# Performance work log

Measured on AMD Instinct MI355X. Metric: run time of the kernel, lower is better.

## Reference

```python
import jax, jax.numpy as jnp
import numpy as np

EMBED_DIM = 1024
NUM_HEADS = 16
HEAD_DIM = EMBED_DIM // NUM_HEADS


def setup_inputs() -> dict:
    key = jax.random.key(0)
    k1, k2, k3, k4, k5 = jax.random.split(key, 5)
    B, S, D = 2, 2048, EMBED_DIM
    s_in = 1.0 / np.sqrt(D)
    x = jax.random.normal(k1, (B, S, D), dtype=jnp.float32)
    W_qkv = jax.random.uniform(k2, (D, 3 * D), dtype=jnp.float32, minval=-s_in, maxval=s_in)
    b_qkv = jax.random.uniform(k3, (3 * D,), dtype=jnp.float32, minval=-s_in, maxval=s_in)
    W_out = jax.random.uniform(k4, (D, D), dtype=jnp.float32, minval=-s_in, maxval=s_in)
    b_out = jax.random.uniform(k5, (D,), dtype=jnp.float32, minval=-s_in, maxval=s_in)
    return {"x": x, "W_qkv": W_qkv, "b_qkv": b_qkv, "W_out": W_out, "b_out": b_out}


def reference(x, W_qkv, b_qkv, W_out, b_out):
    B, S, D = x.shape
    H, Hd = NUM_HEADS, HEAD_DIM
    qkv = x @ W_qkv + b_qkv                      # [B,S,3D]
    qkv = qkv.reshape(B, S, 3, H, Hd)
    q = qkv[:, :, 0].transpose(0, 2, 1, 3)       # [B,H,S,Hd]
    k = qkv[:, :, 1].transpose(0, 2, 1, 3)
    v = qkv[:, :, 2].transpose(0, 2, 1, 3)
    scores = jnp.einsum('bhsd,bhtd->bhst', q, k) / jnp.sqrt(jnp.float32(Hd))
    attn = jax.nn.softmax(scores, axis=-1)       # dropout is identity in eval mode
    out = jnp.einsum('bhst,bhtd->bhsd', attn, v)
    out = out.transpose(0, 2, 1, 3).reshape(B, S, D)
    return out @ W_out + b_out
```

## Files before the change

### kernel.cpp

```cpp
#include <hip/hip_runtime.h>
#include <stdint.h>
#include <math.h>

#define EMBED 1024
#define HEADS 16
#define HDIM  64
#define SEQ   2048
#define BATCH 2

typedef __bf16 bf16x8 __attribute__((ext_vector_type(8)));
typedef float  f32x4  __attribute__((ext_vector_type(4)));
typedef unsigned short u16x8 __attribute__((ext_vector_type(8)));
typedef unsigned short u16x4 __attribute__((ext_vector_type(4)));
typedef uint32_t u32x4v __attribute__((ext_vector_type(4)));

static __device__ __forceinline__ unsigned short f2bf(float f){
  union { float f; uint32_t u; } v; v.f = f;
  uint32_t u = v.u;
  uint32_t r = (u + 0x7FFFu + ((u >> 16) & 1u)) >> 16;
  return (unsigned short)r;
}
static __device__ __forceinline__ bf16x8 as_bf(u16x8 v){ return __builtin_bit_cast(bf16x8, v); }

static __device__ __forceinline__ uint32_t pk_bf16(float a, float b){
#if defined(__has_builtin) && __has_builtin(__builtin_amdgcn_cvt_pk_bf16_f32)
  typedef __bf16 bf16x2 __attribute__((ext_vector_type(2)));
  bf16x2 p = __builtin_amdgcn_cvt_pk_bf16_f32(a, b);
  return __builtin_bit_cast(uint32_t, p);
#else
  return (uint32_t)f2bf(a) | ((uint32_t)f2bf(b) << 16);
#endif
}

static __device__ __forceinline__ float fexp2(float x){
#if defined(__has_builtin) && __has_builtin(__builtin_amdgcn_exp2f)
  return __builtin_amdgcn_exp2f(x);
#else
  return exp2f(x);
#endif
}

static __device__ __forceinline__ void stage16(const unsigned short* gp,
                                               unsigned short* lp_wave, int lane){
#if defined(__has_builtin) && __has_builtin(__builtin_amdgcn_global_load_lds)
  __builtin_amdgcn_global_load_lds((const __attribute__((address_space(1))) void*)gp,
                                   (__attribute__((address_space(3))) void*)lp_wave,
                                   16, 0, 0);
#else
  *(u16x8*)(lp_wave + lane * 8) = *(const u16x8*)gp;
#endif
}

__global__ __launch_bounds__(256) void prep(
    const float* __restrict__ x,      unsigned short* __restrict__ xb,
    const float* __restrict__ W_qkv,  unsigned short* __restrict__ wqkvT,
    const float* __restrict__ W_out,  unsigned short* __restrict__ woutT)
{
  __shared__ unsigned short T[32 * 36];
  const int bid = blockIdx.x;
  const int t   = threadIdx.x;

  if (bid < 4096){
    int i = (bid * 256 + t) * 4;
    float4 v = *(const float4*)(x + i);
    u16x4 o;
    o[0] = f2bf(v.x); o[1] = f2bf(v.y); o[2] = f2bf(v.z); o[3] = f2bf(v.w);
    *(u16x4*)(xb + i) = o;
    return;
  }
  const float* W; unsigned short* Wt; int N, n0, k0;
  if (bid < 7168){
    int idx = bid - 4096;
    W = W_qkv; Wt = wqkvT; N = 3072;
    n0 = (idx % 96) * 32; k0 = (idx / 96) * 32;
  } else {
    int idx = bid - 7168;
    W = W_out; Wt = woutT; N = 1024;
    n0 = (idx & 31) * 32; k0 = (idx >> 5) * 32;
  }
  int kr = t >> 3, nc = (t & 7) * 4;
  float4 wv = *(const float4*)(W + (size_t)(k0 + kr) * N + n0 + nc);
  T[(nc + 0) * 36 + kr] = f2bf(wv.x);
  T[(nc + 1) * 36 + kr] = f2bf(wv.y);
  T[(nc + 2) * 36 + kr] = f2bf(wv.z);
  T[(nc + 3) * 36 + kr] = f2bf(wv.w);
  __syncthreads();
  int nr = t >> 3, kc = (t & 7) * 4;
  *(u16x4*)(Wt + (size_t)(n0 + nr) * 1024 + k0 + kc) = *(const u16x4*)&T[nr * 36 + kc];
}

__global__ __launch_bounds__(256) void vtrans(const unsigned short* __restrict__ V,
                                              unsigned short* __restrict__ VT){
  __shared__ unsigned short T[32 * 36];
  int t = threadIdx.x;
  int s0 = blockIdx.x * 32, d0 = blockIdx.y * 32;
  size_t base = (size_t)blockIdx.z * SEQ * HDIM;
  int sr = t >> 3, dc = (t & 7) * 4;
  u16x4 vv = *(const u16x4*)(V + base + (size_t)(s0 + sr) * HDIM + d0 + dc);
  T[(dc + 0) * 36 + sr] = vv[0];
  T[(dc + 1) * 36 + sr] = vv[1];
  T[(dc + 2) * 36 + sr] = vv[2];
  T[(dc + 3) * 36 + sr] = vv[3];
  __syncthreads();
  int dr = t >> 3, sc = (t & 7) * 4;
  int pos = (((sc >> 2) & 3) << 3) + (((sc >> 4) & 1) << 2);
  *(u16x4*)(VT + base + (size_t)(d0 + dr) * SEQ + s0 + pos) = *(const u16x4*)&T[dr * 36 + sc];
}

__global__ __launch_bounds__(256) void gemm_qkv(
    const unsigned short* __restrict__ A,
    const unsigned short* __restrict__ Bt,
    const float* __restrict__ bias,
    unsigned short* __restrict__ q_ws,
    unsigned short* __restrict__ k_ws,
    unsigned short* __restrict__ v_ws,
    int M, int N, int K)
{
  __shared__ unsigned short As[128 * 32];
  __shared__ unsigned short Bs[128 * 32];
  const int tid  = threadIdx.x;
  const int bm   = blockIdx.x, bn = blockIdx.y;
  const int w    = tid >> 6, lane = tid & 63;
  const int quad = lane >> 4, l16 = lane & 15;
  const int wm   = (w >> 1) * 64, wn = (w & 1) * 64;

  f32x4 acc[4][4] = {};

  for (int k0 = 0; k0 < K; k0 += 32) {
    #pragma unroll
    for (int i = 0; i < 2; i++){
      int c = w + i * 4;
      int row = c * 16 + (lane >> 2);
      int kg = (lane & 3) ^ (row & 3);
      stage16(A  + (size_t)(bm * 128 + row) * K + k0 + kg * 8, &As[c * 512], lane);
      stage16(Bt + (size_t)(bn * 128 + row) * K + k0 + kg * 8, &Bs[c * 512], lane);
    }
    __syncthreads();

    bf16x8 af[4], bfr[4];
    #pragma unroll
    for (int t = 0; t < 4; t++){
      int ra = wm + t * 16 + l16;
      int rb = wn + t * 16 + l16;
      af[t]  = as_bf(*(const u16x8*)&As[(ra << 5) + ((quad ^ (ra & 3)) << 3)]);
      bfr[t] = as_bf(*(const u16x8*)&Bs[(rb << 5) + ((quad ^ (rb & 3)) << 3)]);
    }
    #pragma unroll
    for (int mt = 0; mt < 4; mt++)
      #pragma unroll
      for (int nt = 0; nt < 4; nt++)
        acc[mt][nt] = __builtin_amdgcn_mfma_f32_16x16x32_bf16(af[mt], bfr[nt], acc[mt][nt], 0, 0, 0);
    __syncthreads();
  }

  const int which = (bn * 128) >> 10;
  unsigned short* dst = (which == 0) ? q_ws : (which == 1) ? k_ws : v_ws;
  const float scale = (which == 0) ? 0.18033688f : 1.0f;
  const int b = bm >> 4;
  #pragma unroll
  for (int nt = 0; nt < 4; nt++){
    int gnb = bn * 128 + wn + nt * 16;
    int h   = (gnb & 1023) >> 6;
    int hd  = (gnb & 63) + l16;
    float bv = bias[gnb + l16];
    unsigned short* dp = dst + (size_t)(b * HEADS + h) * SEQ * HDIM + hd;
    #pragma unroll
    for (int mt = 0; mt < 4; mt++){
      int s0 = ((bm & 15) * 128) + wm + mt * 16 + quad * 4;
      #pragma unroll
      for (int r = 0; r < 4; r++)
        dp[(size_t)(s0 + r) * HDIM] = f2bf((acc[mt][nt][r] + bv) * scale);
    }
  }
}

__global__ __launch_bounds__(256) void gemm_out(
    const unsigned short* __restrict__ A,
    const unsigned short* __restrict__ Bt,
    const float* __restrict__ bias,
    float* __restrict__ Cout,
    int M, int N, int K)
{
  __shared__ unsigned short As[128 * 32];
  __shared__ unsigned short Bs[64 * 32];
  const int tid  = threadIdx.x;
  const int bm   = blockIdx.x, bn = blockIdx.y;
  const int w    = tid >> 6, lane = tid & 63;
  const int quad = lane >> 4, l16 = lane & 15;
  const int wm   = (w >> 1) * 64, wn = (w & 1) * 32;

  f32x4 acc[4][2] = {};

  for (int k0 = 0; k0 < K; k0 += 32) {
    #pragma unroll
    for (int i = 0; i < 2; i++){
      int c = w + i * 4;
      int row = c * 16 + (lane >> 2);
      int kg = (lane & 3) ^ (row & 3);
      stage16(A + (size_t)(bm * 128 + row) * K + k0 + kg * 8, &As[c * 512], lane);
    }
    {
      int c = w;
      int row = c * 16 + (lane >> 2);
      int kg = (lane & 3) ^ (row & 3);
      stage16(Bt + (size_t)(bn * 64 + row) * K + k0 + kg * 8, &Bs[c * 512], lane);
    }
    __syncthreads();

    bf16x8 af[4], bfr[2];
    #pragma unroll
    for (int t = 0; t < 4; t++){
      int ra = wm + t * 16 + l16;
      af[t] = as_bf(*(const u16x8*)&As[(ra << 5) + ((quad ^ (ra & 3)) << 3)]);
    }
    #pragma unroll
    for (int t = 0; t < 2; t++){
      int rb = wn + t * 16 + l16;
      bfr[t] = as_bf(*(const u16x8*)&Bs[(rb << 5) + ((quad ^ (rb & 3)) << 3)]);
    }
    #pragma unroll
    for (int mt = 0; mt < 4; mt++)
      #pragma unroll
      for (int nt = 0; nt < 2; nt++)
        acc[mt][nt] = __builtin_amdgcn_mfma_f32_16x16x32_bf16(af[mt], bfr[nt], acc[mt][nt], 0, 0, 0);
    __syncthreads();
  }

  #pragma unroll
  for (int mt = 0; mt < 4; mt++)
    #pragma unroll
    for (int nt = 0; nt < 2; nt++)
      #pragma unroll
      for (int r = 0; r < 4; r++){
        int gm = bm * 128 + wm + mt * 16 + quad * 4 + r;
        int gn = bn * 64 + wn + nt * 16 + l16;
        Cout[(size_t)gm * N + gn] = acc[mt][nt][r] + bias[gn];
      }
}

__global__ __launch_bounds__(512, 1) void attn(
    const unsigned short* __restrict__ q_ws,
    const unsigned short* __restrict__ k_ws,
    const unsigned short* __restrict__ vt_ws,
    unsigned short* __restrict__ o_ws)
{
  __shared__ unsigned short Qs[256 * 64];
  __shared__ unsigned short Ks[2][64 * 64];
  __shared__ unsigned short VTs[2][64 * 64];
  const int tid  = threadIdx.x;
  const int wgid = blockIdx.x;
  const int lin  = (wgid & 7) * 32 + (wgid >> 3);
  const int bh   = lin >> 3, qt = lin & 7;
  const int w    = tid >> 6, lane = tid & 63;
  const int quad = lane >> 4, l16 = lane & 15;
  const size_t base = (size_t)bh * SEQ * HDIM;

  #pragma unroll
  for (int i = 0; i < 4; i++){
    int c = w * 4 + i;
    int row = c * 8 + (lane >> 3);
    int kg = (lane & 7) ^ (row & 7);
    stage16(q_ws + base + (size_t)(qt * 256 + row) * HDIM + kg * 8, &Qs[c * 512], lane);
  }

  const int srow = w * 8 + (lane >> 3);
  const int skg  = (lane & 7) ^ (srow & 7);
  const int dofs = w * 512 + lane * 8;

  stage16(k_ws  + base + (size_t)srow * HDIM + skg * 8, &Ks[0][w * 512],  lane);
  stage16(vt_ws + base + (size_t)srow * SEQ + skg * 8,  &VTs[0][w * 512], lane);
  __syncthreads();

  bf16x8 bq[2][2];
  #pragma unroll
  for (int mq = 0; mq < 2; mq++){
    int row = w * 32 + mq * 16 + l16;
    #pragma unroll
    for (int ks = 0; ks < 2; ks++)
      bq[mq][ks] = as_bf(*(const u16x8*)&Qs[(row << 6) + ((((ks << 2) + quad) ^ (row & 7)) << 3)]);
  }

  const unsigned short* kp = k_ws  + base + (size_t)(64 + srow) * HDIM + skg * 8;
  const unsigned short* vp = vt_ws + base + (size_t)srow * SEQ + 64 + skg * 8;

  f32x4 acc[2][4] = {};
  float li[2] = {0.f, 0.f};

  for (int kt2 = 0; kt2 < SEQ / 128; kt2++){
    #pragma unroll
    for (int half = 0; half < 2; half++){
      const int cur = half;
      const int kt  = kt2 * 2 + half;
      u16x8 kpre, vpre;
      if (kt < SEQ / 64 - 1){
        kpre = *(const u16x8*)kp;  kp += 64 * HDIM;
        vpre = *(const u16x8*)vp;  vp += 64;
      }

      bf16x8 ak[2][4];
      #pragma unroll
      for (int ks = 0; ks < 2; ks++)
        #pragma unroll
        for (int nt = 0; nt < 4; nt++){
          int rk = nt * 16 + l16;
          ak[ks][nt] = as_bf(*(const u16x8*)&Ks[cur][(rk << 6) + ((((ks << 2) + quad) ^ (rk & 7)) << 3)]);
        }
      f32x4 sf[4][2] = {};
      #pragma unroll
      for (int ks = 0; ks < 2; ks++)
        #pragma unroll
        for (int nt = 0; nt < 4; nt++)
          #pragma unroll
          for (int mq = 0; mq < 2; mq++)
            sf[nt][mq] = __builtin_amdgcn_mfma_f32_16x16x32_bf16(ak[ks][nt], bq[mq][ks], sf[nt][mq], 0, 0, 0);

      bf16x8 bv[2][4];
      #pragma unroll
      for (int c = 0; c < 2; c++)
        #pragma unroll
        for (int nt = 0; nt < 4; nt++){
          int rv = nt * 16 + l16;
          bv[c][nt] = as_bf(*(const u16x8*)&VTs[cur][(rv << 6) + ((((c << 2) + quad) ^ (rv & 7)) << 3)]);
        }

      #pragma unroll
      for (int nt = 0; nt < 4; nt++)
        #pragma unroll
        for (int mq = 0; mq < 2; mq++)
          #pragma unroll
          for (int r = 0; r < 4; r++)
            sf[nt][mq][r] = fexp2(sf[nt][mq][r]);
      #pragma unroll
      for (int mq = 0; mq < 2; mq++)
        #pragma unroll
        for (int nt = 0; nt < 4; nt++)
          li[mq] += (sf[nt][mq][0] + sf[nt][mq][1]) + (sf[nt][mq][2] + sf[nt][mq][3]);

      #pragma unroll
      for (int c = 0; c < 2; c++){
        bf16x8 ap[2];
        #pragma unroll
        for (int mq = 0; mq < 2; mq++){
          u32x4v aw;
          aw[0] = pk_bf16(sf[c * 2][mq][0],     sf[c * 2][mq][1]);
          aw[1] = pk_bf16(sf[c * 2][mq][2],     sf[c * 2][mq][3]);
          aw[2] = pk_bf16(sf[c * 2 + 1][mq][0], sf[c * 2 + 1][mq][1]);
          aw[3] = pk_bf16(sf[c * 2 + 1][mq][2], sf[c * 2 + 1][mq][3]);
          ap[mq] = __builtin_bit_cast(bf16x8, aw);
        }
        #pragma unroll
        for (int nt = 0; nt < 4; nt++)
          #pragma unroll
          for (int mq = 0; mq < 2; mq++)
            acc[mq][nt] = __builtin_amdgcn_mfma_f32_16x16x32_bf16(ap[mq], bv[c][nt], acc[mq][nt], 0, 0, 0);
      }

      if (kt < SEQ / 64 - 1){
        *(u16x8*)&Ks[cur ^ 1][dofs]  = kpre;
        *(u16x8*)&VTs[cur ^ 1][dofs] = vpre;
      }
      __syncthreads();
    }
  }

  #pragma unroll
  for (int mq = 0; mq < 2; mq++){
    li[mq] += __shfl_xor(li[mq], 16);
    li[mq] += __shfl_xor(li[mq], 32);
  }
  float inv[2] = {1.0f / li[0], 1.0f / li[1]};
  float invr[2][4];
  #pragma unroll
  for (int mq = 0; mq < 2; mq++)
    #pragma unroll
    for (int r = 0; r < 4; r++)
      invr[mq][r] = __shfl(inv[mq], quad * 4 + r);

  int b = bh >> 4, h = bh & 15;
  #pragma unroll
  for (int mq = 0; mq < 2; mq++)
    #pragma unroll
    for (int nt = 0; nt < 4; nt++)
      #pragma unroll
      for (int r = 0; r < 4; r++){
        int s = qt * 256 + w * 32 + mq * 16 + quad * 4 + r;
        int d = h * 64 + nt * 16 + l16;
        o_ws[((size_t)(b * SEQ + s)) * EMBED + d] = f2bf(acc[mq][nt][r] * invr[mq][r]);
      }
}

extern "C" void kernel_launch(void* const* d_in, const int* in_sizes, int n_in,
                              void* d_out, int out_size, void* d_ws, size_t ws_size,
                              hipStream_t stream) {
  const float* x     = (const float*)d_in[0];
  const float* W_qkv = (const float*)d_in[1];
  const float* b_qkv = (const float*)d_in[2];
  const float* W_out = (const float*)d_in[3];
  const float* b_out = (const float*)d_in[4];
  float* out = (float*)d_out;

  char* ws = (char*)d_ws;
  unsigned short* xb    = (unsigned short*)(ws);
  unsigned short* vt    = (unsigned short*)(ws);
  unsigned short* q     = (unsigned short*)(ws + ((size_t)8  << 20));
  unsigned short* k     = (unsigned short*)(ws + ((size_t)16 << 20));
  unsigned short* v     = (unsigned short*)(ws + ((size_t)24 << 20));
  unsigned short* o     = (unsigned short*)(ws + ((size_t)24 << 20));
  unsigned short* wqkvT = (unsigned short*)(ws + ((size_t)32 << 20));
  unsigned short* woutT = (unsigned short*)(ws + ((size_t)38 << 20));

  prep<<<dim3(8192), dim3(256), 0, stream>>>(x, xb, W_qkv, wqkvT, W_out, woutT);

  gemm_qkv<<<dim3(32, 24), dim3(256), 0, stream>>>(
      xb, wqkvT, b_qkv, q, k, v, 4096, 3072, 1024);

  vtrans<<<dim3(64, 2, 32), dim3(256), 0, stream>>>(v, vt);

  attn<<<dim3(256), dim3(512), 0, stream>>>(q, k, vt, o);

  gemm_out<<<dim3(32, 16), dim3(256), 0, stream>>>(
      o, woutT, b_out, out, 4096, 1024, 1024);
}
```

Baseline: 196.5 us.

## Split attention KV loop across wave pairs with direct global loads

The attention kernel drops its LDS staging of Q, K and V^T and its per-tile barriers. Each wave now loads its MFMA fragments straight from global memory, relying on cache reuse. Pairs of waves split the key tiles by parity and merge partial accumulators and row sums through a small LDS buffer at the end. The grid doubles to 512 blocks of 128 query rows, and launch bounds allow more resident blocks. This trades LDS reuse and explicit prefetch for more parallelism and no synchronisation, at the risk of redundant, less coalesced global or L2 traffic.

```diff
diff --git a/kernel.cpp b/kernel.cpp
--- a/kernel.cpp
+++ b/kernel.cpp
@@ -238,130 +238,120 @@
       }
 }
 
-__global__ __launch_bounds__(512, 1) void attn(
+__global__ __launch_bounds__(512, 4) void attn(
     const unsigned short* __restrict__ q_ws,
     const unsigned short* __restrict__ k_ws,
     const unsigned short* __restrict__ vt_ws,
     unsigned short* __restrict__ o_ws)
 {
-  __shared__ unsigned short Qs[256 * 64];
-  __shared__ unsigned short Ks[2][64 * 64];
-  __shared__ unsigned short VTs[2][64 * 64];
+  __shared__ float CB[34][4][64];
   const int tid  = threadIdx.x;
   const int wgid = blockIdx.x;
-  const int lin  = (wgid & 7) * 32 + (wgid >> 3);
-  const int bh   = lin >> 3, qt = lin & 7;
+  const int lin  = (wgid & 7) * 64 + (wgid >> 3);
+  const int bh   = lin >> 4, qt = lin & 15;
   const int w    = tid >> 6, lane = tid & 63;
   const int quad = lane >> 4, l16 = lane & 15;
+  const int wq   = w >> 1;
+  const int ph   = w & 1;
   const size_t base = (size_t)bh * SEQ * HDIM;
-
-  #pragma unroll
-  for (int i = 0; i < 4; i++){
-    int c = w * 4 + i;
-    int row = c * 8 + (lane >> 3);
-    int kg = (lane & 7) ^ (row & 7);
-    stage16(q_ws + base + (size_t)(qt * 256 + row) * HDIM + kg * 8, &Qs[c * 512], lane);
-  }
-
-  const int srow = w * 8 + (lane >> 3);
-  const int skg  = (lane & 7) ^ (srow & 7);
-  const int dofs = w * 512 + lane * 8;
-
-  stage16(k_ws  + base + (size_t)srow * HDIM + skg * 8, &Ks[0][w * 512],  lane);
-  stage16(vt_ws + base + (size_t)srow * SEQ + skg * 8,  &VTs[0][w * 512], lane);
-  __syncthreads();
+  const int qrow0 = qt * 128 + wq * 32;
 
   bf16x8 bq[2][2];
   #pragma unroll
-  for (int mq = 0; mq < 2; mq++){
-    int row = w * 32 + mq * 16 + l16;
+  for (int mq = 0; mq < 2; mq++)
     #pragma unroll
     for (int ks = 0; ks < 2; ks++)
-      bq[mq][ks] = as_bf(*(const u16x8*)&Qs[(row << 6) + ((((ks << 2) + quad) ^ (row & 7)) << 3)]);
-  }
-
-  const unsigned short* kp = k_ws  + base + (size_t)(64 + srow) * HDIM + skg * 8;
-  const unsigned short* vp = vt_ws + base + (size_t)srow * SEQ + 64 + skg * 8;
+      bq[mq][ks] = as_bf(*(const u16x8*)(q_ws + base +
+                     (size_t)(qrow0 + mq * 16 + l16) * HDIM + (ks * 4 + quad) * 8));
 
   f32x4 acc[2][4] = {};
   float li[2] = {0.f, 0.f};
 
-  for (int kt2 = 0; kt2 < SEQ / 128; kt2++){
-    #pragma unroll
-    for (int half = 0; half < 2; half++){
-      const int cur = half;
-      const int kt  = kt2 * 2 + half;
-      u16x8 kpre, vpre;
-      if (kt < SEQ / 64 - 1){
-        kpre = *(const u16x8*)kp;  kp += 64 * HDIM;
-        vpre = *(const u16x8*)vp;  vp += 64;
-      }
-
-      bf16x8 ak[2][4];
-      #pragma unroll
-      for (int ks = 0; ks < 2; ks++)
-        #pragma unroll
-        for (int nt = 0; nt < 4; nt++){
-          int rk = nt * 16 + l16;
-          ak[ks][nt] = as_bf(*(const u16x8*)&Ks[cur][(rk << 6) + ((((ks << 2) + quad) ^ (rk & 7)) << 3)]);
-        }
-      f32x4 sf[4][2] = {};
-      #pragma unroll
-      for (int ks = 0; ks < 2; ks++)
-        #pragma unroll
-        for (int nt = 0; nt < 4; nt++)
-          #pragma unroll
-          for (int mq = 0; mq < 2; mq++)
-            sf[nt][mq] = __builtin_amdgcn_mfma_f32_16x16x32_bf16(ak[ks][nt], bq[mq][ks], sf[nt][mq], 0, 0, 0);
-
-      bf16x8 bv[2][4];
-      #pragma unroll
-      for (int c = 0; c < 2; c++)
-        #pragma unroll
-        for (int nt = 0; nt < 4; nt++){
-          int rv = nt * 16 + l16;
-          bv[c][nt] = as_bf(*(const u16x8*)&VTs[cur][(rv << 6) + ((((c << 2) + quad) ^ (rv & 7)) << 3)]);
-        }
-
+  for (int t = ph; t < SEQ / 64; t += 2){
+    const unsigned short* kb = k_ws  + base + (size_t)t * 64 * HDIM;
+    const unsigned short* vb = vt_ws + base + t * 64;
+
+    bf16x8 ak[2][4];
+    #pragma unroll
+    for (int ks = 0; ks < 2; ks++)
+      #pragma unroll
+      for (int nt = 0; nt < 4; nt++)
+        ak[ks][nt] = as_bf(*(const u16x8*)(kb +
+                       (size_t)(nt * 16 + l16) * HDIM + (ks * 4 + quad) * 8));
+
+    f32x4 sf[4][2] = {};
+    #pragma unroll
+    for (int ks = 0; ks < 2; ks++)
       #pragma unroll
       for (int nt = 0; nt < 4; nt++)
         #pragma unroll
         for (int mq = 0; mq < 2; mq++)
-          #pragma unroll
-          for (int r = 0; r < 4; r++)
-            sf[nt][mq][r] = fexp2(sf[nt][mq][r]);
+          sf[nt][mq] = __builtin_amdgcn_mfma_f32_16x16x32_bf16(ak[ks][nt], bq[mq][ks], sf[nt][mq], 0, 0, 0);
+
+    bf16x8 bv[2][4];
+    #pragma unroll
+    for (int c = 0; c < 2; c++)
+      #pragma unroll
+      for (int nt = 0; nt < 4; nt++)
+        bv[c][nt] = as_bf(*(const u16x8*)(vb +
+                      (size_t)(nt * 16 + l16) * SEQ + (c * 4 + quad) * 8));
+
+    #pragma unroll
+    for (int nt = 0; nt < 4; nt++)
       #pragma unroll
       for (int mq = 0; mq < 2; mq++)
         #pragma unroll
-        for (int nt = 0; nt < 4; nt++)
-          li[mq] += (sf[nt][mq][0] + sf[nt][mq][1]) + (sf[nt][mq][2] + sf[nt][mq][3]);
-
-      #pragma unroll
-      for (int c = 0; c < 2; c++){
-        bf16x8 ap[2];
+        for (int r = 0; r < 4; r++)
+          sf[nt][mq][r] = fexp2(sf[nt][mq][r]);
+    #pragma unroll
+    for (int mq = 0; mq < 2; mq++)
+      #pragma unroll
+      for (int nt = 0; nt < 4; nt++)
+        li[mq] += (sf[nt][mq][0] + sf[nt][mq][1]) + (sf[nt][mq][2] + sf[nt][mq][3]);
+
+    #pragma unroll
+    for (int c = 0; c < 2; c++){
+      bf16x8 ap[2];
+      #pragma unroll
+      for (int mq = 0; mq < 2; mq++){
+        u32x4v aw;
+        aw[0] = pk_bf16(sf[c * 2][mq][0],     sf[c * 2][mq][1]);
+        aw[1] = pk_bf16(sf[c * 2][mq][2],     sf[c * 2][mq][3]);
+        aw[2] = pk_bf16(sf[c * 2 + 1][mq][0], sf[c * 2 + 1][mq][1]);
+        aw[3] = pk_bf16(sf[c * 2 + 1][mq][2], sf[c * 2 + 1][mq][3]);
+        ap[mq] = __builtin_bit_cast(bf16x8, aw);
+      }
+      #pragma unroll
+      for (int nt = 0; nt < 4; nt++)
         #pragma unroll
-        for (int mq = 0; mq < 2; mq++){
-          u32x4v aw;
-          aw[0] = pk_bf16(sf[c * 2][mq][0],     sf[c * 2][mq][1]);
-          aw[1] = pk_bf16(sf[c * 2][mq][2],     sf[c * 2][mq][3]);
-          aw[2] = pk_bf16(sf[c * 2 + 1][mq][0], sf[c * 2 + 1][mq][1]);
-          aw[3] = pk_bf16(sf[c * 2 + 1][mq][2], sf[c * 2 + 1][mq][3]);
-          ap[mq] = __builtin_bit_cast(bf16x8, aw);
-        }
+        for (int mq = 0; mq < 2; mq++)
+          acc[mq][nt] = __builtin_amdgcn_mfma_f32_16x16x32_bf16(ap[mq], bv[c][nt], acc[mq][nt], 0, 0, 0);
+    }
+  }
+
+  if (ph == 1){
+    #pragma unroll
+    for (int mq = 0; mq < 2; mq++)
+      #pragma unroll
+      for (int nt = 0; nt < 4; nt++)
         #pragma unroll
-        for (int nt = 0; nt < 4; nt++)
-          #pragma unroll
-          for (int mq = 0; mq < 2; mq++)
-            acc[mq][nt] = __builtin_amdgcn_mfma_f32_16x16x32_bf16(ap[mq], bv[c][nt], acc[mq][nt], 0, 0, 0);
-      }
-
-      if (kt < SEQ / 64 - 1){
-        *(u16x8*)&Ks[cur ^ 1][dofs]  = kpre;
-        *(u16x8*)&VTs[cur ^ 1][dofs] = vpre;
-      }
-      __syncthreads();
-    }
-  }
+        for (int r = 0; r < 4; r++)
+          CB[(mq * 4 + nt) * 4 + r][wq][lane] = acc[mq][nt][r];
+    CB[32][wq][lane] = li[0];
+    CB[33][wq][lane] = li[1];
+  }
+  __syncthreads();
+  if (ph == 1) return;
+
+  #pragma unroll
+  for (int mq = 0; mq < 2; mq++)
+    #pragma unroll
+    for (int nt = 0; nt < 4; nt++)
+      #pragma unroll
+      for (int r = 0; r < 4; r++)
+        acc[mq][nt][r] += CB[(mq * 4 + nt) * 4 + r][wq][lane];
+  li[0] += CB[32][wq][lane];
+  li[1] += CB[33][wq][lane];
 
   #pragma unroll
   for (int mq = 0; mq < 2; mq++){
@@ -383,7 +373,7 @@
     for (int nt = 0; nt < 4; nt++)
       #pragma unroll
       for (int r = 0; r < 4; r++){
-        int s = qt * 256 + w * 32 + mq * 16 + quad * 4 + r;
+        int s = qrow0 + mq * 16 + quad * 4 + r;
         int d = h * 64 + nt * 16 + l16;
         o_ws[((size_t)(b * SEQ + s)) * EMBED + d] = f2bf(acc[mq][nt][r] * invr[mq][r]);
       }
@@ -416,7 +406,7 @@
 
   vtrans<<<dim3(64, 2, 32), dim3(256), 0, stream>>>(v, vt);
 
-  attn<<<dim3(256), dim3(512), 0, stream>>>(q, k, vt, o);
+  attn<<<dim3(512), dim3(512), 0, stream>>>(q, k, vt, o);
 
   gemm_out<<<dim3(32, 16), dim3(256), 0, stream>>>(
       o, woutT, b_out, out, 4096, 1024, 1024);
```

Result: slower. 264.7 us (+34.7%).
